# Optimization experiments

Hardware: AMD Instinct MI355X
Metric: run time of the kernel (lower is better)

The kernel has to match this reference:

```python
import jax, jax.numpy as jnp
import numpy as np

POOLED = 7      # kernel_size
SCALE = 0.25    # spatial_scale
GMAX = 2        # upper bound of adaptive sampling grid (box sizes chosen so ceil(roi/7) <= 2)


def setup_inputs() -> dict:
    key = jax.random.key(0)
    k1, k2, k3, k4, k5, k6 = jax.random.split(key, 6)
    B, C, H, W, K = 4, 256, 128, 128, 1000
    features = jax.random.normal(k1, (B, C, H, W), dtype=jnp.float32)
    img = H / SCALE  # 512.0: image-space extent
    bidx = jax.random.randint(k2, (K,), 0, B).astype(jnp.float32)
    bw = jax.random.uniform(k3, (K,), minval=8.0, maxval=56.0)
    bh = jax.random.uniform(k4, (K,), minval=8.0, maxval=56.0)
    x1 = jax.random.uniform(k5, (K,), minval=0.0, maxval=img - 56.0)
    y1 = jax.random.uniform(k6, (K,), minval=0.0, maxval=img - 56.0)
    boxes = jnp.stack([bidx, x1, y1, x1 + bw, y1 + bh], axis=1)
    return {"features": features, "boxes": boxes}


def _sample_coords(start, bin_sz, grid):
    # start/bin_sz/grid: [K] -> coords [K, POOLED, GMAX]
    p = jnp.arange(POOLED, dtype=jnp.float32)
    i = jnp.arange(GMAX, dtype=jnp.float32)
    return (start[:, None, None] + p[None, :, None] * bin_sz[:, None, None]
            + (i[None, None, :] + 0.5) * bin_sz[:, None, None] / grid[:, None, None])


def roi_align(features, boxes):
    B, C, H, W = features.shape
    K = boxes.shape[0]
    b = boxes[:, 0].astype(jnp.int32)
    x1, y1, x2, y2 = (boxes[:, i] * SCALE for i in (1, 2, 3, 4))
    # aligned=False: no -0.5 offset, clamp roi size to >= 1
    roi_w = jnp.maximum(x2 - x1, 1.0)
    roi_h = jnp.maximum(y2 - y1, 1.0)
    bin_w = roi_w / POOLED
    bin_h = roi_h / POOLED
    # sampling_ratio = -1 -> adaptive grid = ceil(roi_size / pooled)
    gh = jnp.ceil(roi_h / POOLED)
    gw = jnp.ceil(roi_w / POOLED)

    y = _sample_coords(y1, bin_h, gh)  # [K,7,GMAX]
    x = _sample_coords(x1, bin_w, gw)  # [K,7,GMAX]
    vy = (jnp.arange(GMAX)[None, None, :] < gh[:, None, None])  # [K,1,GMAX]
    vx = (jnp.arange(GMAX)[None, None, :] < gw[:, None, None])

    # full sample grid [K, 7, GMAX, 7, GMAX] -> flatten to [K, P]
    shp = (K, POOLED, GMAX, POOLED, GMAX)
    Y = jnp.broadcast_to(y[:, :, :, None, None], shp).reshape(K, -1)
    X = jnp.broadcast_to(x[:, None, None, :, :], shp).reshape(K, -1)
    V = jnp.broadcast_to(vy[:, :, :, None, None] & vx[:, None, None, :, :], shp).reshape(K, -1)

    # bilinear interpolation, torchvision boundary semantics
    inval = (Y < -1.0) | (Y > H) | (X < -1.0) | (X > W)
    Yc = jnp.clip(Y, 0.0)
    Xc = jnp.clip(X, 0.0)
    yl = jnp.minimum(Yc.astype(jnp.int32), H - 1)
    xl = jnp.minimum(Xc.astype(jnp.int32), W - 1)
    yh = jnp.minimum(yl + 1, H - 1)
    xh = jnp.minimum(xl + 1, W - 1)
    Yc = jnp.where(yl >= H - 1, yl.astype(jnp.float32), Yc)
    Xc = jnp.where(xl >= W - 1, xl.astype(jnp.float32), Xc)
    ly = Yc - yl
    lx = Xc - xl
    hy = 1.0 - ly
    hx = 1.0 - lx
    m = jnp.where(inval | (~V), 0.0, 1.0)
    w1 = hy * hx * m; w2 = hy * lx * m; w3 = ly * hx * m; w4 = ly * lx * m

    def gather(yi, xi):
        # advanced indexing: [K,P] indices -> [K,P,C]
        return features[b[:, None], :, yi, xi]

    val = (w1[..., None] * gather(yl, xl) + w2[..., None] * gather(yl, xh)
           + w3[..., None] * gather(yh, xl) + w4[..., None] * gather(yh, xh))  # [K,P,C]
    val = val.reshape(K, POOLED, GMAX, POOLED, GMAX, C)
    out = val.sum(axis=(2, 4)) / (gh * gw)[:, None, None, None]  # [K,7,7,C]
    return jnp.transpose(out, (0, 3, 1, 2))  # [K,C,7,7]


def reference(features, boxes):
    return roi_align(features, boxes)
```

## Files before the change

kernel.cpp:

```cpp
#include <hip/hip_runtime.h>

#define POOLED 7
#define SCALE  0.25f
#define CCH    256
#define HH     128
#define WW     128
#define HW     (HH * WW)

#define NCH      16
#define NCHUNK   2
#define NBLK_PER_BOX (CCH / (NCH * NCHUNK))
#define PATCH_H  15
#define PATCH_W  16
#define PIXROW   17
#define NPIX     (14 * PIXROW + 16)
#define CHPAD    20

__global__ __launch_bounds__(256) void roi_align_kernel(
    const float* __restrict__ feat,
    const float* __restrict__ boxes,
    float* __restrict__ out,
    int K)
{
    __shared__ float patch[NPIX * CHPAD];

    int bx = blockIdx.x;
    int k  = bx >> 3;
    int cb = (bx & 7) * (NCH * NCHUNK);
    if (k >= K) return;
    int t = threadIdx.x;

    const float* box = boxes + (size_t)k * 5;
    int   b  = (int)box[0];
    float x1 = box[1] * SCALE;
    float y1 = box[2] * SCALE;
    float x2 = box[3] * SCALE;
    float y2 = box[4] * SCALE;

    float roi_w = fmaxf(x2 - x1, 1.0f);
    float roi_h = fmaxf(y2 - y1, 1.0f);
    float bin_w = roi_w * (1.0f / POOLED);
    float bin_h = roi_h * (1.0f / POOLED);
    int gw = (int)ceilf(roi_w * (1.0f / POOLED));
    int gh = (int)ceilf(roi_h * (1.0f / POOLED));
    float inv_gh = 1.0f / (float)gh;
    float inv_gw = 1.0f / (float)gw;
    int ns = gh * gw;

    float ymin = y1 + 0.5f * bin_h * inv_gh;
    float ymax = y1 + 6 * bin_h + ((gh - 1) + 0.5f) * bin_h * inv_gh;
    float xmin = x1 + 0.5f * bin_w * inv_gw;

    int ylo = min((int)fmaxf(ymin, 0.0f), HH - 1);
    int xlo = min((int)fmaxf(xmin, 0.0f), WW - 1);
    int ylmax = min((int)fmaxf(ymax, 0.0f), HH - 1);
    int h_p = min(ylmax + 1, HH - 1) - ylo + 1;
    if (h_p > PATCH_H) h_p = PATCH_H;

    int p  = t & 63;
    int pc = min(p, 48);
    int pw = pc % POOLED;
    int ph = pc / POOLED;
    int c4 = t >> 6;

    float wa[4], wb[4], wc_[4], wd[4];
    int   oa[4], ob[4], oc[4], od[4];

#pragma unroll
    for (int s = 0; s < 4; ++s) {
        if (s >= ns) break;
        int iy = s % gh;
        int ix = s / gh;

        float y = y1 + ph * bin_h + (iy + 0.5f) * bin_h * inv_gh;
        float x = x1 + pw * bin_w + (ix + 0.5f) * bin_w * inv_gw;
        bool valid = (y >= -1.0f) && (y <= (float)HH) && (x >= -1.0f) && (x <= (float)WW);

        float yc = fmaxf(y, 0.0f);
        int yl = min((int)yc, HH - 1);
        int yh2 = min(yl + 1, HH - 1);
        float ly = (yl >= HH - 1) ? 0.0f : (yc - (float)yl);
        float hy = 1.0f - ly;

        float xc = fmaxf(x, 0.0f);
        int xl = min((int)xc, WW - 1);
        int xh2 = min(xl + 1, WW - 1);
        float lx = (xl >= WW - 1) ? 0.0f : (xc - (float)xl);
        float hx = 1.0f - lx;

        float m = valid ? 1.0f : 0.0f;
        wa[s]  = hy * hx * m;
        wb[s]  = hy * lx * m;
        wc_[s] = ly * hx * m;
        wd[s]  = ly * lx * m;

        int ry  = max(0, min(yl  - ylo, h_p - 1));
        int ryh = max(0, min(yh2 - ylo, h_p - 1));
        int rxl = max(0, min(xl  - xlo, PATCH_W - 1));
        int rxh = max(0, min(xh2 - xlo, PATCH_W - 1));
        oa[s] = (ry  * PIXROW + rxl) * CHPAD;
        ob[s] = (ry  * PIXROW + rxh) * CHPAD;
        oc[s] = (ryh * PIXROW + rxl) * CHPAD;
        od[s] = (ryh * PIXROW + rxh) * CHPAD;
    }

    int lch  = t >> 4;
    int lcol = t & 15;
    int xcol = min(xlo + lcol, WW - 1);
    float sc = inv_gh * inv_gw;

    for (int ch = 0; ch < NCHUNK; ++ch) {
        if (ch) __syncthreads();

        {
            const float* g = feat + ((size_t)b * CCH + cb + ch * NCH + lch) * HW + xcol;
            float* lp = patch + lcol * CHPAD + lch;
            for (int r = 0; r < h_p; ++r) {
                lp[r * (PIXROW * CHPAD)] = g[(ylo + r) * WW];
            }
        }
        __syncthreads();

        if (p < 49) {
            float4 acc = {0.0f, 0.0f, 0.0f, 0.0f};
            const float* cp = patch + c4 * 4;
#pragma unroll
            for (int s = 0; s < 4; ++s) {
                if (s >= ns) break;
                float4 va = *(const float4*)(cp + oa[s]);
                float4 vb = *(const float4*)(cp + ob[s]);
                float4 vc = *(const float4*)(cp + oc[s]);
                float4 vd = *(const float4*)(cp + od[s]);
                float w1 = wa[s], w2 = wb[s], w3 = wc_[s], w4 = wd[s];
                acc.x += w1 * va.x + w2 * vb.x + w3 * vc.x + w4 * vd.x;
                acc.y += w1 * va.y + w2 * vb.y + w3 * vc.y + w4 * vd.y;
                acc.z += w1 * va.z + w2 * vb.z + w3 * vc.z + w4 * vd.z;
                acc.w += w1 * va.w + w2 * vb.w + w3 * vc.w + w4 * vd.w;
            }
            float* obase = out + ((size_t)k * CCH + cb + ch * NCH + c4 * 4) * 49 + p;
            obase[0]      = acc.x * sc;
            obase[49]     = acc.y * sc;
            obase[2 * 49] = acc.z * sc;
            obase[3 * 49] = acc.w * sc;
        }
    }
}

extern "C" void kernel_launch(void* const* d_in, const int* in_sizes, int n_in,
                              void* d_out, int out_size, void* d_ws, size_t ws_size,
                              hipStream_t stream) {
    const float* feat  = (const float*)d_in[0];
    const float* boxes = (const float*)d_in[1];
    float* out = (float*)d_out;

    int K = in_sizes[1] / 5;
    int blocks = K * NBLK_PER_BOX;
    roi_align_kernel<<<blocks, 256, 0, stream>>>(feat, boxes, out, K);
}
```

Baseline: 133.4 us.

## Swizzle shared-memory patch layout, double chunks per block, use nontemporal output stores

Each block now handles four 16-channel chunks instead of two, halving the block count and the per-box setup work repeated across blocks. The shared patch stores each pixel's four float4 channel groups in a rotated slot order based on pixel index, which is meant to cut LDS bank conflicts on the scattered writes and the float4 reads. Output stores become nontemporal so the streamed results skip the cache. Fewer blocks lowers parallelism and lengthens the serial chunk loop in each block.

```diff
diff --git a/kernel.cpp b/kernel.cpp
--- a/kernel.cpp
+++ b/kernel.cpp
@@ -8,7 +8,7 @@
 #define HW     (HH * WW)
 
 #define NCH      16
-#define NCHUNK   2
+#define NCHUNK   4
 #define NBLK_PER_BOX (CCH / (NCH * NCHUNK))
 #define PATCH_H  15
 #define PATCH_W  16
@@ -25,8 +25,8 @@
     __shared__ float patch[NPIX * CHPAD];
 
     int bx = blockIdx.x;
-    int k  = bx >> 3;
-    int cb = (bx & 7) * (NCH * NCHUNK);
+    int k  = bx >> 2;
+    int cb = (bx & 3) * (NCH * NCHUNK);
     if (k >= K) return;
     int t = threadIdx.x;
 
@@ -98,15 +98,21 @@
         int ryh = max(0, min(yh2 - ylo, h_p - 1));
         int rxl = max(0, min(xl  - xlo, PATCH_W - 1));
         int rxh = max(0, min(xh2 - xlo, PATCH_W - 1));
-        oa[s] = (ry  * PIXROW + rxl) * CHPAD;
-        ob[s] = (ry  * PIXROW + rxh) * CHPAD;
-        oc[s] = (ryh * PIXROW + rxl) * CHPAD;
-        od[s] = (ryh * PIXROW + rxh) * CHPAD;
+        int pa = ry  * PIXROW + rxl;
+        int pb = ry  * PIXROW + rxh;
+        int pcx = ryh * PIXROW + rxl;
+        int pd = ryh * PIXROW + rxh;
+        oa[s] = pa  * CHPAD + (((c4 + (pa  >> 3)) & 3) << 2);
+        ob[s] = pb  * CHPAD + (((c4 + (pb  >> 3)) & 3) << 2);
+        oc[s] = pcx * CHPAD + (((c4 + (pcx >> 3)) & 3) << 2);
+        od[s] = pd  * CHPAD + (((c4 + (pd  >> 3)) & 3) << 2);
     }
 
     int lch  = t >> 4;
     int lcol = t & 15;
     int xcol = min(xlo + lcol, WW - 1);
+    int slot = lch >> 2;
+    int jj   = lch & 3;
     float sc = inv_gh * inv_gw;
 
     for (int ch = 0; ch < NCHUNK; ++ch) {
@@ -114,23 +120,23 @@
 
         {
             const float* g = feat + ((size_t)b * CCH + cb + ch * NCH + lch) * HW + xcol;
-            float* lp = patch + lcol * CHPAD + lch;
             for (int r = 0; r < h_p; ++r) {
-                lp[r * (PIXROW * CHPAD)] = g[(ylo + r) * WW];
+                int pix = r * PIXROW + lcol;
+                int a = pix * CHPAD + (((slot + (pix >> 3)) & 3) << 2) + jj;
+                patch[a] = g[(ylo + r) * WW];
             }
         }
         __syncthreads();
 
         if (p < 49) {
             float4 acc = {0.0f, 0.0f, 0.0f, 0.0f};
-            const float* cp = patch + c4 * 4;
 #pragma unroll
             for (int s = 0; s < 4; ++s) {
                 if (s >= ns) break;
-                float4 va = *(const float4*)(cp + oa[s]);
-                float4 vb = *(const float4*)(cp + ob[s]);
-                float4 vc = *(const float4*)(cp + oc[s]);
-                float4 vd = *(const float4*)(cp + od[s]);
+                float4 va = *(const float4*)(patch + oa[s]);
+                float4 vb = *(const float4*)(patch + ob[s]);
+                float4 vc = *(const float4*)(patch + oc[s]);
+                float4 vd = *(const float4*)(patch + od[s]);
                 float w1 = wa[s], w2 = wb[s], w3 = wc_[s], w4 = wd[s];
                 acc.x += w1 * va.x + w2 * vb.x + w3 * vc.x + w4 * vd.x;
                 acc.y += w1 * va.y + w2 * vb.y + w3 * vc.y + w4 * vd.y;
@@ -138,10 +144,10 @@
                 acc.w += w1 * va.w + w2 * vb.w + w3 * vc.w + w4 * vd.w;
             }
             float* obase = out + ((size_t)k * CCH + cb + ch * NCH + c4 * 4) * 49 + p;
-            obase[0]      = acc.x * sc;
-            obase[49]     = acc.y * sc;
-            obase[2 * 49] = acc.z * sc;
-            obase[3 * 49] = acc.w * sc;
+            __builtin_nontemporal_store(acc.x * sc, obase);
+            __builtin_nontemporal_store(acc.y * sc, obase + 49);
+            __builtin_nontemporal_store(acc.z * sc, obase + 2 * 49);
+            __builtin_nontemporal_store(acc.w * sc, obase + 3 * 49);
         }
     }
 }
```

Result: slower. 155.8 us (+16.9%).

## Precompute deduplicated bilinear tap lists per box in a separate prep kernel

Applied to the files above, without the earlier changes.

Adds a prep kernel that computes, for each box and output bin, the bilinear sample taps once, merges taps that hit the same patch pixel, folds in the averaging scale, and writes them to workspace. The gather kernel loads these precomputed (offset, weight) entries instead of recomputing weights per block. Each tap then needs one float4 LDS read and four FMAs, and redundant corner reads are removed. The cost is an extra kernel launch, workspace traffic for the entries, and more registers for the 12-entry array.

```diff
diff --git a/kernel.cpp b/kernel.cpp
--- a/kernel.cpp
+++ b/kernel.cpp
@@ -15,20 +15,17 @@
 #define PIXROW   17
 #define NPIX     (14 * PIXROW + 16)
 #define CHPAD    20
-
-__global__ __launch_bounds__(256) void roi_align_kernel(
-    const float* __restrict__ feat,
-    const float* __restrict__ boxes,
-    float* __restrict__ out,
-    int K)
+#define MAXE     12
+
+struct BoxMeta { int b, ylo, xlo, h_p, mmax, pad0, pad1, pad2; };
+
+__global__ __launch_bounds__(64) void roi_prep(
+    const float* __restrict__ boxes, int K,
+    BoxMeta* __restrict__ meta, int2* __restrict__ ent)
 {
-    __shared__ float patch[NPIX * CHPAD];
-
-    int bx = blockIdx.x;
-    int k  = bx >> 3;
-    int cb = (bx & 7) * (NCH * NCHUNK);
+    int k = blockIdx.x;
     if (k >= K) return;
-    int t = threadIdx.x;
+    int p = threadIdx.x;
 
     const float* box = boxes + (size_t)k * 5;
     int   b  = (int)box[0];
@@ -46,6 +43,7 @@
     float inv_gh = 1.0f / (float)gh;
     float inv_gw = 1.0f / (float)gw;
     int ns = gh * gw;
+    float sc = inv_gh * inv_gw;
 
     float ymin = y1 + 0.5f * bin_h * inv_gh;
     float ymax = y1 + 6 * bin_h + ((gh - 1) + 0.5f) * bin_h * inv_gh;
@@ -57,18 +55,15 @@
     int h_p = min(ylmax + 1, HH - 1) - ylo + 1;
     if (h_p > PATCH_H) h_p = PATCH_H;
 
-    int p  = t & 63;
     int pc = min(p, 48);
     int pw = pc % POOLED;
     int ph = pc / POOLED;
-    int c4 = t >> 6;
-
-    float wa[4], wb[4], wc_[4], wd[4];
-    int   oa[4], ob[4], oc[4], od[4];
-
-#pragma unroll
-    for (int s = 0; s < 4; ++s) {
-        if (s >= ns) break;
+
+    int   offs[MAXE];
+    float ws[MAXE];
+    int m = 0;
+
+    for (int s = 0; s < ns; ++s) {
         int iy = s % gh;
         int ix = s / gh;
 
@@ -88,36 +83,86 @@
         float lx = (xl >= WW - 1) ? 0.0f : (xc - (float)xl);
         float hx = 1.0f - lx;
 
-        float m = valid ? 1.0f : 0.0f;
-        wa[s]  = hy * hx * m;
-        wb[s]  = hy * lx * m;
-        wc_[s] = ly * hx * m;
-        wd[s]  = ly * lx * m;
+        float mk = valid ? 1.0f : 0.0f;
 
         int ry  = max(0, min(yl  - ylo, h_p - 1));
         int ryh = max(0, min(yh2 - ylo, h_p - 1));
         int rxl = max(0, min(xl  - xlo, PATCH_W - 1));
         int rxh = max(0, min(xh2 - xlo, PATCH_W - 1));
-        oa[s] = (ry  * PIXROW + rxl) * CHPAD;
-        ob[s] = (ry  * PIXROW + rxh) * CHPAD;
-        oc[s] = (ryh * PIXROW + rxl) * CHPAD;
-        od[s] = (ryh * PIXROW + rxh) * CHPAD;
+
+        int   co[4] = { (ry  * PIXROW + rxl) * CHPAD, (ry  * PIXROW + rxh) * CHPAD,
+                        (ryh * PIXROW + rxl) * CHPAD, (ryh * PIXROW + rxh) * CHPAD };
+        float cw[4] = { hy * hx * mk, hy * lx * mk, ly * hx * mk, ly * lx * mk };
+
+        for (int c = 0; c < 4; ++c) {
+            int o = co[c];
+            float w = cw[c];
+            bool found = false;
+            for (int j = 0; j < m; ++j) {
+                if (offs[j] == o) { ws[j] += w; found = true; break; }
+            }
+            if (!found && m < MAXE) { offs[m] = o; ws[m] = w; ++m; }
+        }
+    }
+
+    if (p >= 49) m = 0;
+    for (int j = 0; j < m; ++j) ws[j] *= sc;
+    for (int j = m; j < MAXE; ++j) { offs[j] = 0; ws[j] = 0.0f; }
+
+    int mm = m;
+    for (int d = 1; d < 64; d <<= 1) mm = max(mm, __shfl_xor(mm, d));
+
+    if (p == 0) {
+        BoxMeta mt; mt.b = b; mt.ylo = ylo; mt.xlo = xlo; mt.h_p = h_p;
+        mt.mmax = mm; mt.pad0 = mt.pad1 = mt.pad2 = 0;
+        meta[k] = mt;
+    }
+
+    int2* eb = ent + (size_t)k * MAXE * 64 + p;
+    for (int j = 0; j < MAXE; ++j)
+        eb[j * 64] = make_int2(offs[j], __float_as_int(ws[j]));
+}
+
+__global__ __launch_bounds__(256) void roi_gather(
+    const float* __restrict__ feat,
+    const BoxMeta* __restrict__ meta,
+    const int2* __restrict__ ent,
+    float* __restrict__ out, int K)
+{
+    __shared__ float patch[NPIX * CHPAD];
+
+    int bx = blockIdx.x;
+    int k  = bx >> 3;
+    int cb = (bx & 7) * (NCH * NCHUNK);
+    if (k >= K) return;
+    int t = threadIdx.x;
+    int p  = t & 63;
+    int c4 = t >> 6;
+
+    BoxMeta mt = meta[k];
+    int mmax = mt.mmax;
+
+    int2 e[MAXE];
+    const int2* eb = ent + (size_t)k * MAXE * 64 + p;
+#pragma unroll
+    for (int j = 0; j < MAXE; ++j) {
+        if (j >= mmax) break;
+        e[j] = eb[j * 64];
     }
 
     int lch  = t >> 4;
     int lcol = t & 15;
-    int xcol = min(xlo + lcol, WW - 1);
-    float sc = inv_gh * inv_gw;
+    int xcol = min(mt.xlo + lcol, WW - 1);
+    int h_p  = mt.h_p;
 
     for (int ch = 0; ch < NCHUNK; ++ch) {
         if (ch) __syncthreads();
 
         {
-            const float* g = feat + ((size_t)b * CCH + cb + ch * NCH + lch) * HW + xcol;
+            const float* g = feat + ((size_t)mt.b * CCH + cb + ch * NCH + lch) * HW + xcol;
             float* lp = patch + lcol * CHPAD + lch;
-            for (int r = 0; r < h_p; ++r) {
-                lp[r * (PIXROW * CHPAD)] = g[(ylo + r) * WW];
-            }
+            for (int r = 0; r < h_p; ++r)
+                lp[r * (PIXROW * CHPAD)] = g[(mt.ylo + r) * WW];
         }
         __syncthreads();
 
@@ -125,23 +170,20 @@
             float4 acc = {0.0f, 0.0f, 0.0f, 0.0f};
             const float* cp = patch + c4 * 4;
 #pragma unroll
-            for (int s = 0; s < 4; ++s) {
-                if (s >= ns) break;
-                float4 va = *(const float4*)(cp + oa[s]);
-                float4 vb = *(const float4*)(cp + ob[s]);
-                float4 vc = *(const float4*)(cp + oc[s]);
-                float4 vd = *(const float4*)(cp + od[s]);
-                float w1 = wa[s], w2 = wb[s], w3 = wc_[s], w4 = wd[s];
-                acc.x += w1 * va.x + w2 * vb.x + w3 * vc.x + w4 * vd.x;
-                acc.y += w1 * va.y + w2 * vb.y + w3 * vc.y + w4 * vd.y;
-                acc.z += w1 * va.z + w2 * vb.z + w3 * vc.z + w4 * vd.z;
-                acc.w += w1 * va.w + w2 * vb.w + w3 * vc.w + w4 * vd.w;
+            for (int j = 0; j < MAXE; ++j) {
+                if (j >= mmax) break;
+                float4 v = *(const float4*)(cp + e[j].x);
+                float w = __int_as_float(e[j].y);
+                acc.x += w * v.x;
+                acc.y += w * v.y;
+                acc.z += w * v.z;
+                acc.w += w * v.w;
             }
             float* obase = out + ((size_t)k * CCH + cb + ch * NCH + c4 * 4) * 49 + p;
-            obase[0]      = acc.x * sc;
-            obase[49]     = acc.y * sc;
-            obase[2 * 49] = acc.z * sc;
-            obase[3 * 49] = acc.w * sc;
+            obase[0]      = acc.x;
+            obase[49]     = acc.y;
+            obase[2 * 49] = acc.z;
+            obase[3 * 49] = acc.w;
         }
     }
 }
@@ -154,6 +196,11 @@
     float* out = (float*)d_out;
 
     int K = in_sizes[1] / 5;
-    int blocks = K * NBLK_PER_BOX;
-    roi_align_kernel<<<blocks, 256, 0, stream>>>(feat, boxes, out, K);
+
+    size_t meta_bytes = ((size_t)K * sizeof(BoxMeta) + 255) & ~(size_t)255;
+    BoxMeta* meta = (BoxMeta*)d_ws;
+    int2* ent = (int2*)((char*)d_ws + meta_bytes);
+
+    roi_prep<<<K, 64, 0, stream>>>(boxes, K, meta, ent);
+    roi_gather<<<K * NBLK_PER_BOX, 256, 0, stream>>>(feat, meta, ent, out, K);
 }
```

Result: slower. 214.1 us (+60.6%).
